# Optimization experiments

Hardware: AMD Instinct MI355X
Metric: run time of the kernel (lower is better)

The kernel has to match this reference:

```python
import jax, jax.numpy as jnp
import numpy as np

MAX_REL = 11  # hardcoded max_relative_position in the module
BN_EPS = 1e-5


def _wn_linear(x, v, g):
    # torch weight_norm on Conv2d 1x1 (dim=0): w = g * v / ||v||_row
    w = v * (g / jnp.linalg.norm(v, axis=1))[:, None]
    return x @ w.T


def _rel_embed(table, lq, lk):
    dist = jnp.arange(lk)[None, :] - jnp.arange(lq)[:, None]
    idx = jnp.clip(dist, -MAX_REL, MAX_REL) + MAX_REL
    return table[idx]  # [lq, lk, d_k]


def setup_inputs() -> dict:
    key = jax.random.key(0)
    B, N, L, D, H = 32, 325, 12, 128, 8
    dk = D // H
    ks = jax.random.split(key, 12)
    rn = lambda k, s, sc=1.0: jax.random.normal(k, s, jnp.float32) * sc
    wq_v = rn(ks[0], (D, D), 1.0 / np.sqrt(D))
    wk_v = rn(ks[1], (D, D), 1.0 / np.sqrt(D))
    wv_v = rn(ks[2], (D, D), 1.0 / np.sqrt(D))
    fc_v = rn(ks[3], (D, D), 1.0 / np.sqrt(D))
    nrm = lambda v: jnp.linalg.norm(v, axis=1)  # weight_norm init: g = ||v||
    return {
        "input_Q": rn(ks[4], (B, N, L, D)),
        "input_K": rn(ks[5], (B, N, L, D)),
        "input_V": rn(ks[6], (B, N, L, D)),
        "wq_v": wq_v, "wq_g": nrm(wq_v),
        "wk_v": wk_v, "wk_g": nrm(wk_v),
        "wv_v": wv_v, "wv_g": nrm(wv_v),
        "fc_v": fc_v, "fc_g": nrm(fc_v),
        "rel_k": rn(ks[7], (2 * MAX_REL + 1, dk), np.sqrt(2.0 / (2 * MAX_REL + 1 + dk)) * np.sqrt(2.0)),
        "rel_v": rn(ks[8], (2 * MAX_REL + 1, dk), np.sqrt(2.0 / (2 * MAX_REL + 1 + dk)) * np.sqrt(2.0)),
        "w1": rn(ks[9], (H, H), np.sqrt(2.0 / H)),
        "w2": rn(ks[10], (H, H), np.sqrt(2.0 / H)),
        "bn_gamma": jnp.ones((D,), jnp.float32),
        "bn_beta": jnp.zeros((D,), jnp.float32),
    }


def reference(input_Q, input_K, input_V, wq_v, wq_g, wk_v, wk_g, wv_v, wv_g,
              fc_v, fc_g, rel_k, rel_v, w1, w2, bn_gamma, bn_beta):
    B, N, L, D = input_Q.shape
    H = w1.shape[0]
    dk = D // H
    scale = 1.0 / np.sqrt(dk)

    Q = _wn_linear(input_Q, wq_v, wq_g).reshape(B, N, L, H, dk)
    K = _wn_linear(input_K, wk_v, wk_g).reshape(B, N, L, H, dk)
    V = _wn_linear(input_V, wv_v, wv_g).reshape(B, N, L, H, dk)

    # content scores + relative-position key scores
    s1 = jnp.einsum('bnqhd,bnkhd->bnhqk', Q, K)
    K2 = _rel_embed(rel_k, L, L)                      # [L, L, dk]
    s2 = jnp.einsum('bnqhd,qkd->bnhqk', Q, K2)
    scores = (s1 + s2) * scale

    # learned cross-head mixing before softmax (w1)
    scores = jnp.einsum('bnhqk,hg->bngqk', scores, w1)
    attn = jax.nn.softmax(jax.nn.leaky_relu(scores, 0.2), axis=-1)
    # learned cross-head mixing after softmax (w2)
    attn = jnp.einsum('bnhqk,hg->bngqk', attn, w2)

    # dual context paths: V and relative-position V
    c1 = jnp.einsum('bnhqk,bnkhd->bnhqd', attn, V)
    V2 = _rel_embed(rel_v, L, L)                      # [L, L, dk]
    c2 = jnp.einsum('bnhqk,qkd->bnhqd', attn, V2)
    ctx = jnp.transpose(c1 + c2, (0, 1, 3, 2, 4)).reshape(B, N, L, D)

    # batch norm over (B, N, L) per channel (stand-in for RepresentativeBatchNorm2d)
    mean = ctx.mean(axis=(0, 1, 2))
    var = ctx.var(axis=(0, 1, 2))
    ctx_n = (ctx - mean) * jax.lax.rsqrt(var + BN_EPS) * bn_gamma + bn_beta

    out = _wn_linear(ctx_n, fc_v, fc_g)
    out = jax.nn.relu(out) + input_V

    attn_ret = jnp.transpose(attn, (3, 0, 1, 2, 4)).reshape(L, B * N * H, L)
    return out, attn_ret
```

## Files before the change

### kernel.cpp

```cpp
#include <hip/hip_runtime.h>
#include <math.h>

#define B_   32
#define N_   325
#define L_   12
#define D_   128
#define H_   8
#define DK_  16
#define BN_  (B_*N_)
#define ROWS_ (BN_*L_)
#define TAB_ 23
#define BNH_ (BN_*H_)
#define OUT_MAIN_ ((size_t)ROWS_ * D_)

#define XS_  136
#define QS2_ 132
#define RS2_ 20
#define PSP_ 148
#define NCMAX_ 64

typedef short v8s __attribute__((ext_vector_type(8)));
typedef float v4f __attribute__((ext_vector_type(4)));

__device__ __forceinline__ unsigned short f2bf_bits(float f) {
    unsigned int u = __float_as_uint(f);
    unsigned int r = (u + 0x7fffu + ((u >> 16) & 1u)) >> 16;
    return (unsigned short)r;
}

__global__ __launch_bounds__(64)
void prep_kernel(const float* __restrict__ wqv, const float* __restrict__ wqg,
                 const float* __restrict__ wkv, const float* __restrict__ wkg,
                 const float* __restrict__ wvv, const float* __restrict__ wvg,
                 const float* __restrict__ fcv, const float* __restrict__ fcg,
                 unsigned short* __restrict__ Wb, float* __restrict__ stats,
                 int statn)
{
    const int b = blockIdx.x, t = threadIdx.x;
    if (b >= 4*D_) {
        const int b0 = (b - 4*D_) * 1024;
        #pragma unroll
        for (int j = 0; j < 16; ++j) {
            const int o = b0 + j*64 + t;
            if (o < statn) stats[o] = 0.f;
        }
        return;
    }
    const int m = b >> 7, o = b & 127;
    const float* v; const float* g;
    if      (m == 0) { v = wqv; g = wqg; }
    else if (m == 1) { v = wkv; g = wkg; }
    else if (m == 2) { v = wvv; g = wvg; }
    else             { v = fcv; g = fcg; }
    float x0 = v[o*D_ + t];
    float x1 = v[o*D_ + t + 64];
    float ss = x0*x0 + x1*x1;
    #pragma unroll
    for (int off = 32; off > 0; off >>= 1) ss += __shfl_down(ss, off, 64);
    ss = __shfl(ss, 0, 64);
    const float scale = g[o] / sqrtf(ss);
    unsigned short* W = Wb + m*(D_*D_);
    {
        int k = t;
        int off = ((o>>4)*4 + (k>>5))*512 + ((k>>3)&3)*128 + (o&15)*8 + (k&7);
        W[off] = f2bf_bits(x0*scale);
        k = t + 64;
        off = ((o>>4)*4 + (k>>5))*512 + ((k>>3)&3)*128 + (o&15)*8 + (k&7);
        W[off] = f2bf_bits(x1*scale);
    }
}

__global__ __launch_bounds__(256, 4)
void attn_kernel(const float* __restrict__ xq, const float* __restrict__ xk,
                 const float* __restrict__ xv,
                 const float* __restrict__ relk, const float* __restrict__ relv,
                 const float* __restrict__ w1g, const float* __restrict__ w2g,
                 const unsigned short* __restrict__ Wb,
                 float* __restrict__ outm, float* __restrict__ attn_out,
                 float* __restrict__ stats, int statmask)
{
    __shared__ __align__(16) char smem[3*16*XS_*2];
    __shared__ __align__(16) float sQ[L_][QS2_];
    __shared__ __align__(16) float sK[L_][QS2_];
    __shared__ __align__(16) float sV[L_][QS2_];
    __shared__ __align__(16) float sRk[TAB_*RS2_];
    __shared__ __align__(16) float sRv[TAB_*RS2_];
    __shared__ float sW1[H_*H_];
    __shared__ float sW2[H_*H_];
    __shared__ float sStats[256];

    unsigned short (*sXb)[16][XS_] =
        reinterpret_cast<unsigned short (*)[16][XS_]>(smem);
    float* pS  = (float*)smem;
    float* pS2 = pS + 8*PSP_;

    const int tid = threadIdx.x;
    const int bn  = blockIdx.x;
    const size_t base = (size_t)bn * (L_*D_);

    {
        const float4* q4 = (const float4*)(xq + base);
        const float4* k4 = (const float4*)(xk + base);
        const float4* v4 = (const float4*)(xv + base);
        for (int idx = tid; idx < 3*384; idx += 256) {
            const int mat = idx / 384;
            const int rem = idx - mat*384;
            const int row = rem >> 5;
            const int c4  = (rem & 31) * 4;
            const float4* s4 = (mat == 0) ? q4 : ((mat == 1) ? k4 : v4);
            float4 v = s4[rem];
            ushort4 u;
            u.x = f2bf_bits(v.x); u.y = f2bf_bits(v.y);
            u.z = f2bf_bits(v.z); u.w = f2bf_bits(v.w);
            *(ushort4*)&sXb[mat][row][c4] = u;
        }
        for (int idx = tid; idx < TAB_*DK_; idx += 256) {
            const int r = idx >> 4, c = idx & 15;
            sRk[r*RS2_ + c] = relk[idx];
            sRv[r*RS2_ + c] = relv[idx];
        }
        if (tid < H_*H_) { sW1[tid] = w1g[tid]; sW2[tid] = w2g[tid]; }
        sStats[tid] = 0.f;
    }
    __syncthreads();

    {
        const int wave = tid >> 6;
        const int lane = tid & 63;
        const int quad = lane >> 4;
        const int c15  = lane & 15;
        const int token0 = quad*4;
        #pragma unroll
        for (int i = 0; i < 6; ++i) {
            const int cb   = wave*6 + i;
            const int mat  = cb >> 3;
            const int tile = cb & 7;
            v8s a[4];
            #pragma unroll
            for (int kk = 0; kk < 4; ++kk)
                a[kk] = *(const v8s*)&sXb[mat][c15][kk*32 + quad*8];
            const v8s* WB = (const v8s*)(Wb + mat*(D_*D_));
            v4f acc = {0.f, 0.f, 0.f, 0.f};
            #pragma unroll
            for (int kk = 0; kk < 4; ++kk) {
                v8s bfrag = WB[(tile*4 + kk)*64 + lane];
                acc = __builtin_amdgcn_mfma_f32_16x16x32_bf16(a[kk], bfrag, acc, 0, 0, 0);
            }
            float (*dst)[QS2_] = (mat == 0) ? sQ : ((mat == 1) ? sK : sV);
            #pragma unroll
            for (int r = 0; r < 4; ++r)
                if (token0 + r < L_)
                    dst[token0 + r][tile*16 + c15] = acc[r];
        }
    }
    __syncthreads();

    for (int task = tid; task < H_*L_*L_; task += 256) {
        const int h = task / 144;
        const int r = task - h*144;
        const int q = r / 12;
        const int k = r - q*12;
        const float* Qp = &sQ[q][h*DK_];
        const float* Kp = &sK[k][h*DK_];
        const float* Rp = &sRk[(k - q + 11)*RS2_];
        float s = 0.f;
        #pragma unroll
        for (int d4 = 0; d4 < 4; ++d4) {
            v4f qv = *(const v4f*)(Qp + d4*4);
            v4f kv = *(const v4f*)(Kp + d4*4);
            v4f rv = *(const v4f*)(Rp + d4*4);
            s += qv.x*(kv.x+rv.x);
            s += qv.y*(kv.y+rv.y);
            s += qv.z*(kv.z+rv.z);
            s += qv.w*(kv.w+rv.w);
        }
        pS[h*PSP_ + r] = s * 0.25f;
    }
    __syncthreads();

    if (tid < H_*L_) {
        const int g = tid / 12;
        const int q = tid - g*12;
        float vals[L_];
        float mx = -1e30f;
        #pragma unroll
        for (int k = 0; k < L_; ++k) {
            float a = 0.f;
            #pragma unroll
            for (int h = 0; h < H_; ++h) a += pS[h*PSP_ + q*12 + k] * sW1[h*H_ + g];
            a = (a >= 0.f) ? a : 0.2f*a;
            vals[k] = a;
            mx = fmaxf(mx, a);
        }
        float sum = 0.f;
        #pragma unroll
        for (int k = 0; k < L_; ++k) { vals[k] = expf(vals[k] - mx); sum += vals[k]; }
        const float inv = 1.f / sum;
        #pragma unroll
        for (int k = 0; k < L_; ++k) pS2[g*PSP_ + q*12 + k] = vals[k]*inv;
    }
    __syncthreads();

    for (int task = tid; task < H_*L_*L_; task += 256) {
        const int g = task / 144;
        const int r = task - g*144;
        const int q = r / 12;
        const int k = r - q*12;
        float a = 0.f;
        #pragma unroll
        for (int h = 0; h < H_; ++h) a += pS2[h*PSP_ + r] * sW2[h*H_ + g];
        pS[g*PSP_ + r] = a;
        attn_out[(size_t)q*((size_t)BNH_*L_) + ((size_t)bn*H_ + g)*L_ + k] = a;
    }
    __syncthreads();

    {
        v4f s4  = {0.f, 0.f, 0.f, 0.f};
        v4f s24 = {0.f, 0.f, 0.f, 0.f};
        const int c4 = tid & 31;
        const int c  = c4 * 4;
        const int h  = c4 >> 2;
        const int dd = c & 15;
        for (int task = tid; task < L_*32; task += 256) {
            const int q = task >> 5;
            const float* Ap = &pS[h*PSP_ + q*12];
            v4f a0 = *(const v4f*)(Ap);
            v4f a1 = *(const v4f*)(Ap + 4);
            v4f a2 = *(const v4f*)(Ap + 8);
            const float av[12] = {a0.x,a0.y,a0.z,a0.w, a1.x,a1.y,a1.z,a1.w,
                                  a2.x,a2.y,a2.z,a2.w};
            v4f acc = {0.f, 0.f, 0.f, 0.f};
            #pragma unroll
            for (int k = 0; k < L_; ++k) {
                const float a = av[k];
                v4f vv = *(const v4f*)&sV[k][c];
                v4f rv = *(const v4f*)&sRv[(k - q + 11)*RS2_ + dd];
                acc.x += a*(vv.x+rv.x);
                acc.y += a*(vv.y+rv.y);
                acc.z += a*(vv.z+rv.z);
                acc.w += a*(vv.w+rv.w);
            }
            *(v4f*)&outm[((size_t)bn*L_ + q)*D_ + c] = acc;
            s4  += acc;
            s24 += acc*acc;
        }
        const int lane = tid & 63;
        #pragma unroll
        for (int j = 0; j < 4; ++j) {
            float a = s4[j]  + __shfl_down(s4[j],  32, 64);
            float b = s24[j] + __shfl_down(s24[j], 32, 64);
            if (lane < 32) {
                atomicAdd(&sStats[c + j],       a);
                atomicAdd(&sStats[128 + c + j], b);
            }
        }
    }
    __syncthreads();
    atomicAdd(&stats[(bn & statmask)*256 + tid], sStats[tid]);
}

__global__ __launch_bounds__(128)
void bnfinal_kernel(const float* __restrict__ stats,
                    const float* __restrict__ gamma, const float* __restrict__ beta,
                    float* __restrict__ stats2, int nc)
{
    const int c = threadIdx.x;
    float s = 0.f, s2 = 0.f;
    for (int j = 0; j < nc; ++j) {
        s  += stats[j*256 + c];
        s2 += stats[j*256 + c + 128];
    }
    const float invn = 1.f / (float)ROWS_;
    float mean = s*invn;
    float var  = s2*invn - mean*mean;
    float sc   = rsqrtf(var + 1e-5f) * gamma[c];
    stats2[c]     = sc;
    stats2[c+128] = beta[c] - mean*sc;
}

__global__ __launch_bounds__(256, 4)
void fc_kernel(float* __restrict__ outm, const float* __restrict__ stats2,
               const unsigned short* __restrict__ Wfc,
               const float* __restrict__ resid)
{
    __shared__ float sSS[256];
    __shared__ __align__(16) unsigned short sC[16][XS_];
    const int tid = threadIdx.x;
    const size_t row0 = (size_t)blockIdx.x * 16;

    sSS[tid] = stats2[tid];
    __syncthreads();
    for (int idx = tid; idx < 16*D_/4; idx += 256) {
        const int r  = idx >> 5;
        const int c4 = (idx & 31) * 4;
        float4 v = *(const float4*)&outm[(row0 + r)*D_ + c4];
        ushort4 u;
        u.x = f2bf_bits(v.x*sSS[c4+0] + sSS[128+c4+0]);
        u.y = f2bf_bits(v.y*sSS[c4+1] + sSS[128+c4+1]);
        u.z = f2bf_bits(v.z*sSS[c4+2] + sSS[128+c4+2]);
        u.w = f2bf_bits(v.w*sSS[c4+3] + sSS[128+c4+3]);
        *(ushort4*)&sC[r][c4] = u;
    }
    __syncthreads();

    const int wave = tid >> 6;
    const int lane = tid & 63;
    const int quad = lane >> 4;
    const int c15  = lane & 15;
    v8s a[4];
    #pragma unroll
    for (int kk = 0; kk < 4; ++kk)
        a[kk] = *(const v8s*)&sC[c15][kk*32 + quad*8];
    const v8s* WB = (const v8s*)Wfc;
    #pragma unroll
    for (int tt = 0; tt < 2; ++tt) {
        const int tile = wave*2 + tt;
        v4f acc = {0.f, 0.f, 0.f, 0.f};
        #pragma unroll
        for (int kk = 0; kk < 4; ++kk) {
            v8s bfrag = WB[(tile*4 + kk)*64 + lane];
            acc = __builtin_amdgcn_mfma_f32_16x16x32_bf16(a[kk], bfrag, acc, 0, 0, 0);
        }
        #pragma unroll
        for (int r = 0; r < 4; ++r) {
            const size_t aidx = (row0 + quad*4 + r)*D_ + tile*16 + c15;
            outm[aidx] = fmaxf(acc[r], 0.f) + resid[aidx];
        }
    }
}

extern "C" void kernel_launch(void* const* d_in, const int* in_sizes, int n_in,
                              void* d_out, int out_size, void* d_ws, size_t ws_size,
                              hipStream_t stream)
{
    const float* xq   = (const float*)d_in[0];
    const float* xk   = (const float*)d_in[1];
    const float* xv   = (const float*)d_in[2];
    const float* wqv  = (const float*)d_in[3];
    const float* wqg  = (const float*)d_in[4];
    const float* wkv  = (const float*)d_in[5];
    const float* wkg  = (const float*)d_in[6];
    const float* wvv  = (const float*)d_in[7];
    const float* wvg  = (const float*)d_in[8];
    const float* fcv  = (const float*)d_in[9];
    const float* fcg  = (const float*)d_in[10];
    const float* relk = (const float*)d_in[11];
    const float* relv = (const float*)d_in[12];
    const float* w1   = (const float*)d_in[13];
    const float* w2   = (const float*)d_in[14];
    const float* gam  = (const float*)d_in[15];
    const float* bet  = (const float*)d_in[16];

    const size_t wboff = 4*D_*D_*sizeof(unsigned short);
    unsigned short* Wb = (unsigned short*)d_ws;

    long avail = (long)((ws_size - wboff) / sizeof(float)) - 256;
    int nc = 1;
    while (nc < NCMAX_ && (long)(nc*2)*256 <= avail) nc *= 2;

    float* stats  = (float*)((char*)d_ws + wboff);
    float* stats2 = stats + (size_t)nc*256;

    float* outm     = (float*)d_out;
    float* attn_out = outm + OUT_MAIN_;

    prep_kernel<<<4*D_ + 16, 64, 0, stream>>>(wqv,wqg, wkv,wkg, wvv,wvg, fcv,fcg,
                                              Wb, stats, nc*256);
    attn_kernel<<<BN_, 256, 0, stream>>>(xq, xk, xv, relk, relv, w1, w2,
                                         Wb, outm, attn_out, stats, nc - 1);
    bnfinal_kernel<<<1, 128, 0, stream>>>(stats, gam, bet, stats2, nc);
    fc_kernel<<<ROWS_/16, 256, 0, stream>>>(outm, stats2, Wb + 3*D_*D_, xv);
}
```

Baseline: 434.8 us.

## Compute attention scores with split-bf16 MFMA instead of scalar fp32 dot products

Q and K projections are stored as hi/lo bf16 pairs so the QK^T and Q·relK score terms can be computed with MFMA instructions, approximating fp32 precision via split-bf16 products. Relative-position scores are computed against the full 23-entry table and then gathered by diagonal through a per-wave scratch buffer. The W1 head-mixing loop is also vectorized, and the stats buffer moves into the reused shared scratch area to cut LDS usage. The extra conversions, scratch traffic and precision changes add risk, and the score stage was a small part of the per-block work.

```diff
diff --git a/kernel.cpp b/kernel.cpp
--- a/kernel.cpp
+++ b/kernel.cpp
@@ -17,6 +17,8 @@
 #define QS2_ 132
 #define RS2_ 20
 #define PSP_ 148
+#define QCS_ 264
+#define RCS_ 40
 #define NCMAX_ 64
 
 typedef short v8s __attribute__((ext_vector_type(8)));
@@ -80,19 +82,19 @@
                  float* __restrict__ stats, int statmask)
 {
     __shared__ __align__(16) char smem[3*16*XS_*2];
-    __shared__ __align__(16) float sQ[L_][QS2_];
-    __shared__ __align__(16) float sK[L_][QS2_];
+    __shared__ __align__(16) unsigned short Qcat[16*QCS_];
+    __shared__ __align__(16) unsigned short Kcat[16*QCS_];
+    __shared__ __align__(16) unsigned short Rcat[24*RCS_];
     __shared__ __align__(16) float sV[L_][QS2_];
-    __shared__ __align__(16) float sRk[TAB_*RS2_];
     __shared__ __align__(16) float sRv[TAB_*RS2_];
     __shared__ float sW1[H_*H_];
     __shared__ float sW2[H_*H_];
-    __shared__ float sStats[256];
 
     unsigned short (*sXb)[16][XS_] =
         reinterpret_cast<unsigned short (*)[16][XS_]>(smem);
-    float* pS  = (float*)smem;
-    float* pS2 = pS + 8*PSP_;
+    float* pS     = (float*)smem;
+    float* pS2    = pS + 8*PSP_;
+    float* sStats = pS + 2*8*PSP_;
 
     const int tid = threadIdx.x;
     const int bn  = blockIdx.x;
@@ -116,11 +118,15 @@
         }
         for (int idx = tid; idx < TAB_*DK_; idx += 256) {
             const int r = idx >> 4, c = idx & 15;
-            sRk[r*RS2_ + c] = relk[idx];
+            float kv = relk[idx];
+            unsigned short hb = f2bf_bits(kv);
+            float hf = __uint_as_float(((unsigned int)hb) << 16);
+            Rcat[r*RCS_ + c]      = hb;
+            Rcat[r*RCS_ + 16 + c] = f2bf_bits(kv - hf);
             sRv[r*RS2_ + c] = relv[idx];
         }
+        if (tid < RCS_) Rcat[23*RCS_ + tid] = 0;
         if (tid < H_*H_) { sW1[tid] = w1g[tid]; sW2[tid] = w2g[tid]; }
-        sStats[tid] = 0.f;
     }
     __syncthreads();
 
@@ -146,48 +152,110 @@
                 v8s bfrag = WB[(tile*4 + kk)*64 + lane];
                 acc = __builtin_amdgcn_mfma_f32_16x16x32_bf16(a[kk], bfrag, acc, 0, 0, 0);
             }
-            float (*dst)[QS2_] = (mat == 0) ? sQ : ((mat == 1) ? sK : sV);
+            if (mat == 2) {
+                #pragma unroll
+                for (int r = 0; r < 4; ++r)
+                    if (token0 + r < L_)
+                        sV[token0 + r][tile*16 + c15] = acc[r];
+            } else {
+                unsigned short* cat = (mat == 0) ? Qcat : Kcat;
+                #pragma unroll
+                for (int r = 0; r < 4; ++r) {
+                    const int token = token0 + r;
+                    if (token < L_) {
+                        float x = acc[r];
+                        unsigned short hb = f2bf_bits(x);
+                        float hf = __uint_as_float(((unsigned int)hb) << 16);
+                        cat[token*QCS_ + tile*32 + c15]      = hb;
+                        cat[token*QCS_ + tile*32 + 16 + c15] = f2bf_bits(x - hf);
+                    }
+                }
+            }
+        }
+    }
+    __syncthreads();
+
+    {
+        const int wave = tid >> 6;
+        const int lane = tid & 63;
+        const int quad = lane >> 4;
+        const int c15  = lane & 15;
+        const unsigned short* zrow = &Rcat[23*RCS_];
+        float* scr = pS2 + wave*276;
+
+        #pragma unroll
+        for (int hh = 0; hh < 2; ++hh) {
+            const int h = wave*2 + hh;
+            v8s a1 = *(const v8s*)&Qcat[c15*QCS_ + h*32 + quad*8];
+            v8s b1 = *(const v8s*)&Kcat[c15*QCS_ + h*32 + (quad&1)*8];
+            const unsigned short* b2p = (quad < 2)
+                ? &Kcat[c15*QCS_ + h*32 + 16 + quad*8]
+                : zrow + (quad&1)*8;
+            v8s b2 = *(const v8s*)b2p;
+            v4f s1 = {0.f, 0.f, 0.f, 0.f};
+            s1 = __builtin_amdgcn_mfma_f32_16x16x32_bf16(a1, b2, s1, 0, 0, 0);
+            s1 = __builtin_amdgcn_mfma_f32_16x16x32_bf16(a1, b1, s1, 0, 0, 0);
+
+            const int j0 = c15;
+            const int j1 = (c15 < 7) ? 16 + c15 : 23;
+            v8s rb1_0 = *(const v8s*)&Rcat[j0*RCS_ + (quad&1)*8];
+            const unsigned short* r2p0 = (quad < 2)
+                ? &Rcat[j0*RCS_ + 16 + quad*8] : zrow + (quad&1)*8;
+            v8s rb2_0 = *(const v8s*)r2p0;
+            v8s rb1_1 = *(const v8s*)&Rcat[j1*RCS_ + (quad&1)*8];
+            const unsigned short* r2p1 = (quad < 2)
+                ? &Rcat[j1*RCS_ + 16 + quad*8] : zrow + (quad&1)*8;
+            v8s rb2_1 = *(const v8s*)r2p1;
+            v4f s20 = {0.f, 0.f, 0.f, 0.f};
+            v4f s21 = {0.f, 0.f, 0.f, 0.f};
+            s20 = __builtin_amdgcn_mfma_f32_16x16x32_bf16(a1, rb2_0, s20, 0, 0, 0);
+            s20 = __builtin_amdgcn_mfma_f32_16x16x32_bf16(a1, rb1_0, s20, 0, 0, 0);
+            s21 = __builtin_amdgcn_mfma_f32_16x16x32_bf16(a1, rb2_1, s21, 0, 0, 0);
+            s21 = __builtin_amdgcn_mfma_f32_16x16x32_bf16(a1, rb1_1, s21, 0, 0, 0);
+
             #pragma unroll
-            for (int r = 0; r < 4; ++r)
-                if (token0 + r < L_)
-                    dst[token0 + r][tile*16 + c15] = acc[r];
-        }
-    }
-    __syncthreads();
-
-    for (int task = tid; task < H_*L_*L_; task += 256) {
-        const int h = task / 144;
-        const int r = task - h*144;
-        const int q = r / 12;
-        const int k = r - q*12;
-        const float* Qp = &sQ[q][h*DK_];
-        const float* Kp = &sK[k][h*DK_];
-        const float* Rp = &sRk[(k - q + 11)*RS2_];
-        float s = 0.f;
-        #pragma unroll
-        for (int d4 = 0; d4 < 4; ++d4) {
-            v4f qv = *(const v4f*)(Qp + d4*4);
-            v4f kv = *(const v4f*)(Kp + d4*4);
-            v4f rv = *(const v4f*)(Rp + d4*4);
-            s += qv.x*(kv.x+rv.x);
-            s += qv.y*(kv.y+rv.y);
-            s += qv.z*(kv.z+rv.z);
-            s += qv.w*(kv.w+rv.w);
-        }
-        pS[h*PSP_ + r] = s * 0.25f;
+            for (int r = 0; r < 4; ++r) {
+                const int q = quad*4 + r;
+                if (q < L_) {
+                    scr[q*23 + j0] = s20[r];
+                    if (c15 < 7) scr[q*23 + 16 + c15] = s21[r];
+                }
+            }
+            asm volatile("s_waitcnt lgkmcnt(0)" ::: "memory");
+            __builtin_amdgcn_sched_barrier(0);
+            if (c15 < L_) {
+                #pragma unroll
+                for (int r = 0; r < 4; ++r) {
+                    const int q = quad*4 + r;
+                    if (q < L_) {
+                        float s2 = scr[q*23 + (c15 - q + 11)];
+                        pS[h*PSP_ + q*12 + c15] = (s1[r] + s2) * 0.25f;
+                    }
+                }
+            }
+        }
     }
     __syncthreads();
 
     if (tid < H_*L_) {
         const int g = tid / 12;
         const int q = tid - g*12;
-        float vals[L_];
+        v4f v0 = {0.f,0.f,0.f,0.f}, v1 = {0.f,0.f,0.f,0.f}, v2 = {0.f,0.f,0.f,0.f};
+        #pragma unroll
+        for (int h = 0; h < H_; ++h) {
+            const float w = sW1[h*H_ + g];
+            const float* row = &pS[h*PSP_ + q*12];
+            v4f r0 = *(const v4f*)(row);
+            v4f r1 = *(const v4f*)(row + 4);
+            v4f r2 = *(const v4f*)(row + 8);
+            v0 += r0*w; v1 += r1*w; v2 += r2*w;
+        }
+        float vals[L_] = {v0.x,v0.y,v0.z,v0.w, v1.x,v1.y,v1.z,v1.w,
+                          v2.x,v2.y,v2.z,v2.w};
         float mx = -1e30f;
         #pragma unroll
         for (int k = 0; k < L_; ++k) {
-            float a = 0.f;
-            #pragma unroll
-            for (int h = 0; h < H_; ++h) a += pS[h*PSP_ + q*12 + k] * sW1[h*H_ + g];
+            float a = vals[k];
             a = (a >= 0.f) ? a : 0.2f*a;
             vals[k] = a;
             mx = fmaxf(mx, a);
@@ -199,6 +267,7 @@
         #pragma unroll
         for (int k = 0; k < L_; ++k) pS2[g*PSP_ + q*12 + k] = vals[k]*inv;
     }
+    sStats[tid] = 0.f;
     __syncthreads();
 
     for (int task = tid; task < H_*L_*L_; task += 256) {
```

Measured after the change: 438.5 us. About the same (+0.9%).
